# Kernel tuning notes

Measured on AMD Instinct MI355X. Metric: run time of the kernel, lower is better.

## Reference

```python
import jax, jax.numpy as jnp
import numpy as np
import math

FS, N_FFT, NUM_BANDS, NUM_BINS = 16000, 512, 31, 257
H = 96  # dim_hidden

def band_partition():
    f_min, f_max = FS / N_FFT, FS / 2.0
    z_min = 69.0 + 12.0 * math.log2(f_min / 440.0)
    z_max = 69.0 + 12.0 * math.log2(f_max / 440.0)
    z = np.linspace(z_min, z_max, NUM_BANDS + 2)
    f_points = 440.0 * 2.0 ** ((z - 69.0) / 12.0)
    bins = np.round(f_points * N_FFT / FS).astype(np.int64)
    bins[0] = 0
    bands = []
    for i in range(NUM_BANDS):
        s = max(0, int(bins[i]))
        e = min(NUM_BINS, int(bins[i + 2]) + 1)
        if e <= s:
            e = s + 1
        bands.append((s, e))
    return bands

BANDS = band_partition()

def hann(L):
    # torch.hann_window default (periodic=True)
    return 0.5 - 0.5 * jnp.cos(2.0 * jnp.pi * jnp.arange(L, dtype=jnp.float32) / L)

def chan_ln(x, eps=1e-5):
    # AdaNorm2d assumed = LayerNorm over channel dim, no affine
    m = jnp.mean(x, axis=1, keepdims=True)
    v = jnp.var(x, axis=1, keepdims=True)
    return (x - m) * jax.lax.rsqrt(v + eps)

def prelu(x, a):
    return jnp.where(x >= 0, x, a * x)

def setup_inputs() -> dict:
    key = jax.random.key(0)
    ks = jax.random.split(key, 20)
    B, T = 4, 1000
    return {
        'mix_repr': jax.random.normal(ks[0], (B, H, NUM_BINS, T), jnp.float32),
        'spin': jax.random.normal(ks[1], (B, 64, NUM_BINS, T), jnp.float32),
        'doa': jax.random.normal(ks[2], (B, 36), jnp.float32),
        'enc_w': jax.random.normal(ks[3], (NUM_BANDS, H, 64), jnp.float32) * 0.05,
        'enc_b': jax.random.normal(ks[4], (NUM_BANDS, H), jnp.float32) * 0.05,
        'enc_a': 0.25 * jnp.ones((NUM_BANDS,), jnp.float32),
        'dqg_w': jax.random.normal(ks[5], (NUM_BANDS, 2 * H, 36), jnp.float32) * 0.05,
        'dqg_b': jax.random.normal(ks[6], (NUM_BANDS, 2 * H), jnp.float32) * 0.05,
        'dec_w': jax.random.normal(ks[7], (NUM_BANDS, H, H), jnp.float32) * 0.05,
        'dec_b': jax.random.normal(ks[8], (NUM_BANDS, H), jnp.float32) * 0.05,
        'dec_a': 0.25 * jnp.ones((NUM_BANDS,), jnp.float32),
        'qw': jax.random.normal(ks[9], (H, H), jnp.float32) * 0.05,
        'qb': jax.random.normal(ks[10], (H,), jnp.float32) * 0.05,
        'kw': jax.random.normal(ks[11], (H, H), jnp.float32) * 0.05,
        'kb': jax.random.normal(ks[12], (H,), jnp.float32) * 0.05,
        'vw': jax.random.normal(ks[13], (H, H), jnp.float32) * 0.05,
        'vb': jax.random.normal(ks[14], (H,), jnp.float32) * 0.05,
        'ow': jax.random.normal(ks[15], (H, H), jnp.float32) * 0.05,
        'ob': jax.random.normal(ks[16], (H,), jnp.float32) * 0.05,
    }

def reference(mix_repr, spin, doa, enc_w, enc_b, enc_a, dqg_w, dqg_b,
              dec_w, dec_b, dec_a, qw, qb, kw, kb, vw, vb, ow, ob):
    B, D, F, T = mix_repr.shape
    merged = jnp.zeros((B, H, F, T), mix_repr.dtype)
    wsum = jnp.zeros((F,), mix_repr.dtype)
    for k, (s, e) in enumerate(BANDS):  # fixed set of 31 static ragged bands
        L = e - s
        win = hann(L)
        sub = spin[:, :, s:e, :]                                   # [B,64,L,T]
        feat = jnp.einsum('oc,bcft->boft', enc_w[k], sub) + enc_b[k][None, :, None, None]
        feat = prelu(chan_ln(feat), enc_a[k])
        qp = doa @ dqg_w[k].T + dqg_b[k]                           # [B,2H]
        gamma, beta = qp[:, :H], qp[:, H:]
        tgt = (1.0 + gamma)[:, :, None, None] * feat + beta[:, :, None, None]
        dec = jnp.einsum('oc,bcft->boft', dec_w[k], tgt) + dec_b[k][None, :, None, None]
        dec = prelu(chan_ln(dec), dec_a[k])
        merged = merged.at[:, :, s:e, :].add(dec * win[None, None, :, None])
        wsum = wsum.at[s:e].add(win)
    merged = merged / jnp.clip(wsum, 1e-8)[None, None, :, None]
    # MixtureQueryFusion: 1x1 conv cross-attention gate
    Q = jnp.einsum('oc,bcft->boft', qw, mix_repr) + qb[None, :, None, None]
    K = jnp.einsum('oc,bcft->boft', kw, merged) + kb[None, :, None, None]
    V = jnp.einsum('oc,bcft->boft', vw, merged) + vb[None, :, None, None]
    attn = jax.nn.sigmoid(jnp.sum(Q * K, axis=1, keepdims=True) / jnp.sqrt(jnp.float32(H)))
    attended = V * attn
    out = mix_repr + jnp.einsum('oc,bcft->boft', ow, attended) + ob[None, :, None, None]
    return out
```

## Files before the change

### kernel.cpp

```cpp
#include <hip/hip_runtime.h>
#include <math.h>

#define NBANDS 31
#define FT 257000

typedef __attribute__((ext_vector_type(8))) short bh8;
typedef __attribute__((ext_vector_type(4))) float f4;

__constant__ int d_bs[NBANDS] = {0,1,1,2,2,2,3,3,4,5,6,7,8,10,11,13,16,19,23,27,32,38,45,54,64,76,91,108,128,152,181};
__constant__ int d_be[NBANDS] = {2,3,3,3,4,4,5,6,7,8,9,11,12,14,17,20,24,28,33,39,46,55,65,77,92,109,129,153,182,216,257};

__device__ __forceinline__ unsigned short b16u(float v) {
  __bf16 h = (__bf16)v;
  return __builtin_bit_cast(unsigned short, h);
}
__device__ __forceinline__ unsigned pk2(float a, float b) {
  return (unsigned)b16u(a) | ((unsigned)b16u(b) << 16);
}
__device__ __forceinline__ float hann1(int i, int L) {
  return 0.5f - 0.5f * cosf(6.283185307179586f * (float)i / (float)L);
}

__global__ __launch_bounds__(256) void prep_w(
    const float* __restrict__ enc_w, const float* __restrict__ dec_w,
    const float* __restrict__ qw, const float* __restrict__ kw,
    const float* __restrict__ vw, const float* __restrict__ ow,
    unsigned short* __restrict__ w16) {
  const int stride = gridDim.x * blockDim.x;
  for (int i = blockIdx.x * blockDim.x + threadIdx.x; i < 513024; i += stride) {
    float v;
    if (i < 190464) {
      const int k = i / 6144, r = i - k * 6144;
      const int tile = r >> 9, li = r & 511;
      const int lane = li >> 3, j = li & 7;
      const int g = lane >> 4, n = lane & 15;
      const int mt = tile >> 1, kt = tile & 1;
      v = enc_w[k * 6144 + (mt * 16 + n) * 64 + kt * 32 + g * 8 + j];
    } else if (i < 476160) {
      const int i2 = i - 190464;
      const int k = i2 / 9216, r = i2 - k * 9216;
      const int tile = r >> 9, li = r & 511;
      const int lane = li >> 3, j = li & 7;
      const int g = lane >> 4, n = lane & 15;
      const int mt = tile / 3, kt = tile - mt * 3;
      v = dec_w[k * 9216 + (mt * 16 + n) * 96 + kt * 32 + g * 8 + j];
    } else {
      const int i2 = i - 476160;
      const int a = i2 / 9216, r = i2 - a * 9216;
      const int tile = r >> 9, li = r & 511;
      const int lane = li >> 3, j = li & 7;
      const int g = lane >> 4, n = lane & 15;
      const int mt = tile / 3, kt = tile - mt * 3;
      const float* src = (a == 0) ? qw : (a == 1) ? kw : (a == 2) ? vw : ow;
      v = src[(mt * 16 + n) * 96 + kt * 32 + g * 8 + j];
    }
    w16[i] = b16u(v);
  }
}

__global__ __launch_bounds__(192) void qp_kernel(const float* __restrict__ doa,
                                                 const float* __restrict__ dqg_w,
                                                 const float* __restrict__ dqg_b,
                                                 float* __restrict__ gbuf) {
  const int k = blockIdx.x, b = blockIdx.y;
  const int tid = threadIdx.x;
  __shared__ float sdoa[36];
  if (tid < 36) sdoa[tid] = doa[b * 36 + tid];
  __syncthreads();
  const float* wr = dqg_w + (k * 192 + tid) * 36;
  float acc = dqg_b[k * 192 + tid];
  #pragma unroll
  for (int i = 0; i < 36; ++i) acc = fmaf(wr[i], sdoa[i], acc);
  if (tid < 96) acc += 1.0f;
  gbuf[(k * 4 + b) * 192 + tid] = acc;
}

__global__ __launch_bounds__(320) void tab_kernel(float* __restrict__ ftab) {
  const int f = blockIdx.x * blockDim.x + threadIdx.x;
  if (f >= 257) return;
  int k0 = 0; while (d_be[k0] <= f) ++k0;
  int k1 = k0; while (k1 < NBANDS && d_bs[k1] <= f) ++k1;
  float wsum = 0.f, wn[5];
  for (int k = k0; k < k1; ++k) {
    const float wv = hann1(f - d_bs[k], d_be[k] - d_bs[k]);
    wn[k - k0] = wv; wsum += wv;
  }
  float* o = ftab + f * 8;
  o[0] = (float)k0; o[1] = (float)(k1 - k0); o[2] = 1.0f / fmaxf(wsum, 1e-8f);
  #pragma unroll
  for (int j = 0; j < 5; ++j) o[3 + j] = (j < k1 - k0) ? wn[j] : 0.f;
}

#define LDSWAIT asm volatile("s_waitcnt lgkmcnt(0)" ::: "memory")

__device__ __forceinline__ void init6(f4* acc, const float* s, int off) {
  #pragma unroll
  for (int mt = 0; mt < 6; ++mt) {
    const float4 bb = *reinterpret_cast<const float4*>(s + mt * 16 + off);
    acc[mt] = (f4){bb.x, bb.y, bb.z, bb.w};
  }
}
__device__ __forceinline__ void ln96(const f4* acc, float& mean, float& rs) {
  float s0 = 0.f, s1 = 0.f, s2 = 0.f, s3 = 0.f;
  float q0 = 0.f, q1 = 0.f, q2 = 0.f, q3 = 0.f;
  #pragma unroll
  for (int mt = 0; mt < 6; ++mt) {
    const float a0 = acc[mt][0], a1 = acc[mt][1], a2 = acc[mt][2], a3 = acc[mt][3];
    s0 += a0; s1 += a1; s2 += a2; s3 += a3;
    q0 = fmaf(a0, a0, q0); q1 = fmaf(a1, a1, q1);
    q2 = fmaf(a2, a2, q2); q3 = fmaf(a3, a3, q3);
  }
  float sm = (s0 + s1) + (s2 + s3);
  float sq = (q0 + q1) + (q2 + q3);
  sm += __shfl_xor(sm, 16); sm += __shfl_xor(sm, 32);
  sq += __shfl_xor(sq, 16); sq += __shfl_xor(sq, 32);
  mean = sm * (1.f / 96.f);
  rs = rsqrtf(sq * (1.f / 96.f) - mean * mean + 1e-5f);
}
__device__ __forceinline__ void load6s(bh8* dst, const unsigned short* p, int step9) {
  #pragma unroll
  for (int mt = 0; mt < 6; ++mt)
    dst[mt] = *reinterpret_cast<const bh8*>(p + ((mt * step9) << 9));
}

__global__ __launch_bounds__(256, 3) void fused_mfma(
    const float* __restrict__ mix, const float* __restrict__ spin,
    const unsigned short* __restrict__ enc16, const float* __restrict__ enc_b, const float* __restrict__ enc_a,
    const unsigned short* __restrict__ dec16, const float* __restrict__ dec_b, const float* __restrict__ dec_a,
    const float* __restrict__ gb, const float* __restrict__ ftab,
    const unsigned short* __restrict__ q16, const float* __restrict__ qb,
    const unsigned short* __restrict__ k16, const float* __restrict__ kb,
    const unsigned short* __restrict__ v16, const float* __restrict__ vb,
    const unsigned short* __restrict__ o16, const float* __restrict__ ob,
    float* __restrict__ out) {
  const int id0 = (int)blockIdx.x;
  const int id  = (id0 & 7) * 2056 + (id0 >> 3);
  const int tt  = id & 15;
  const int fb  = id >> 4;
  const int f   = fb % 257;
  const int b   = fb / 257;
  const int t0  = tt << 6;

  const int tid  = threadIdx.x;
  const int lane = tid & 63;
  const int w    = tid >> 6;
  const int g    = lane >> 4;
  const int n    = lane & 15;
  const int col  = (w << 4) + n;
  const int t    = t0 + col;
  const int tcl  = (t < 1000) ? t : 999;
  const int sw   = (n & 7) << 3;
  const int lb   = lane << 3;

  __shared__ __align__(16) char smem[28160];
  unsigned short* XT = (unsigned short*)smem;
  float* stage = (float*)(smem + 16384);
  float* OS = (float*)smem;
  unsigned short* xw = XT + col * 128;

  const float* ft = ftab + f * 8;
  const int k0 = (int)ft[0];
  const int nb = (int)ft[1];
  const float winv = ft[2];

  {
    const int tot = (nb << 9) + 384;
    for (int i = tid; i < tot; i += 256) {
      const int kk = i >> 9, r = i & 511;
      float v = 0.f;
      if (kk < nb) {
        const int k = k0 + kk;
        if      (r < 96)  v = enc_b[k * 96 + r];
        else if (r < 192) v = dec_b[k * 96 + (r - 96)];
        else if (r < 384) v = gb[(k * 4 + b) * 192 + (r - 192)];
        else if (r == 384) v = enc_a[k];
        else if (r == 385) v = dec_a[k];
        else if (r == 386) v = ft[3 + kk];
      } else {
        const int r2 = i - (nb << 9);
        v = (r2 < 96) ? qb[r2] : (r2 < 192) ? kb[r2 - 96] : (r2 < 288) ? vb[r2 - 192] : ob[r2 - 288];
      }
      stage[i] = v;
    }
  }

  const float* spL = spin + b * 64 * FT + f * 1000 + tcl;
  const float* mxL = mix  + b * 96 * FT + f * 1000 + tcl;

  bh8 spb[2];
  {
    float spf[16];
    #pragma unroll
    for (int j = 0; j < 8; ++j) spf[j]     = __builtin_nontemporal_load(spL + (g * 8 + j) * FT);
    #pragma unroll
    for (int j = 0; j < 8; ++j) spf[8 + j] = __builtin_nontemporal_load(spL + (32 + g * 8 + j) * FT);
    #pragma unroll
    for (int kt = 0; kt < 2; ++kt)
      #pragma unroll
      for (int j = 0; j < 8; ++j) spb[kt][j] = (short)b16u(spf[kt * 8 + j]);
  }

  bh8 pre[6];
  load6s(pre, enc16 + k0 * 6144 + lb, 2);

  __syncthreads();

  f4 macc[6];
  #pragma unroll
  for (int mt = 0; mt < 6; ++mt) macc[mt] = (f4){0.f, 0.f, 0.f, 0.f};

  const int oo = g * 4;

  for (int kk = 0; kk < nb; ++kk) {
    const int k = k0 + kk;
    const unsigned short* ew  = enc16 + k * 6144 + lb;
    const unsigned short* dwp = dec16 + k * 9216 + lb;
    const float* stg = stage + (kk << 9);

    f4 acc[6];
    init6(acc, stg, oo);
    #pragma unroll
    for (int mt = 0; mt < 6; ++mt)
      acc[mt] = __builtin_amdgcn_mfma_f32_16x16x32_bf16(pre[mt], spb[0], acc[mt], 0, 0, 0);
    #pragma unroll
    for (int mt = 0; mt < 6; ++mt) {
      const bh8 af = *reinterpret_cast<const bh8*>(ew + ((mt * 2 + 1) << 9));
      acc[mt] = __builtin_amdgcn_mfma_f32_16x16x32_bf16(af, spb[1], acc[mt], 0, 0, 0);
    }

    load6s(pre, dwp, 3);

    float mean, rs;
    ln96(acc, mean, rs);
    const float ea = stg[384];
    #pragma unroll
    for (int mt = 0; mt < 6; ++mt) {
      const float4 ga = *reinterpret_cast<const float4*>(stg + 192 + mt * 16 + oo);
      const float4 be = *reinterpret_cast<const float4*>(stg + 288 + mt * 16 + oo);
      float x0 = (acc[mt][0] - mean) * rs; x0 = (x0 >= 0.f) ? x0 : ea * x0;
      float x1 = (acc[mt][1] - mean) * rs; x1 = (x1 >= 0.f) ? x1 : ea * x1;
      float x2 = (acc[mt][2] - mean) * rs; x2 = (x2 >= 0.f) ? x2 : ea * x2;
      float x3 = (acc[mt][3] - mean) * rs; x3 = (x3 >= 0.f) ? x3 : ea * x3;
      uint2 u;
      u.x = pk2(fmaf(ga.x, x0, be.x), fmaf(ga.y, x1, be.y));
      u.y = pk2(fmaf(ga.z, x2, be.z), fmaf(ga.w, x3, be.w));
      *reinterpret_cast<uint2*>(xw + ((mt * 16 + g * 4) ^ sw)) = u;
    }
    LDSWAIT;

    f4 dacc[6];
    init6(dacc, stg + 96, oo);
    {
      const bh8 bf0 = *reinterpret_cast<const bh8*>(xw + ((0 * 32 + g * 8) ^ sw));
      #pragma unroll
      for (int mt = 0; mt < 6; ++mt)
        dacc[mt] = __builtin_amdgcn_mfma_f32_16x16x32_bf16(pre[mt], bf0, dacc[mt], 0, 0, 0);
    }

    {
      const bool more = (kk + 1 < nb);
      load6s(pre, more ? (enc16 + (k + 1) * 6144 + lb) : (q16 + lb), more ? 2 : 3);
    }

    #pragma unroll
    for (int kt = 1; kt < 3; ++kt) {
      const bh8 bf = *reinterpret_cast<const bh8*>(xw + ((kt * 32 + g * 8) ^ sw));
      #pragma unroll
      for (int mt = 0; mt < 6; ++mt) {
        const bh8 af = *reinterpret_cast<const bh8*>(dwp + ((mt * 3 + kt) << 9));
        dacc[mt] = __builtin_amdgcn_mfma_f32_16x16x32_bf16(af, bf, dacc[mt], 0, 0, 0);
      }
    }
    float mean2, rs2;
    ln96(dacc, mean2, rs2);
    const float da = stg[385];
    const float win = stg[386];
    #pragma unroll
    for (int mt = 0; mt < 6; ++mt)
      #pragma unroll
      for (int r = 0; r < 4; ++r) {
        float x = (dacc[mt][r] - mean2) * rs2;
        x = (x >= 0.f) ? x : da * x;
        macc[mt][r] = fmaf(win, x, macc[mt][r]);
      }
  }

  float mxf[24];
  #pragma unroll
  for (int kt = 0; kt < 3; ++kt)
    #pragma unroll
    for (int j = 0; j < 8; ++j) mxf[kt * 8 + j] = mxL[(kt * 32 + g * 8 + j) * FT];

  #pragma unroll
  for (int mt = 0; mt < 6; ++mt) {
    uint2 u;
    u.x = pk2(macc[mt][0] * winv, macc[mt][1] * winv);
    u.y = pk2(macc[mt][2] * winv, macc[mt][3] * winv);
    *reinterpret_cast<uint2*>(xw + ((mt * 16 + g * 4) ^ sw)) = u;
  }
  LDSWAIT;
  bh8 gfr[3];
  #pragma unroll
  for (int kt = 0; kt < 3; ++kt) gfr[kt] = *reinterpret_cast<const bh8*>(xw + ((kt * 32 + g * 8) ^ sw));

  bh8 mxb[3];
  #pragma unroll
  for (int kt = 0; kt < 3; ++kt)
    #pragma unroll
    for (int j = 0; j < 8; ++j) mxb[kt][j] = (short)b16u(mxf[kt * 8 + j]);

  const float* stQ = stage + (nb << 9);

  f4 qacc[6];
  init6(qacc, stQ, oo);
  const unsigned short* qp16 = q16 + lb;
  #pragma unroll
  for (int mt = 0; mt < 6; ++mt)
    qacc[mt] = __builtin_amdgcn_mfma_f32_16x16x32_bf16(pre[mt], mxb[0], qacc[mt], 0, 0, 0);
  load6s(pre, k16 + lb, 3);
  #pragma unroll
  for (int kt = 1; kt < 3; ++kt)
    #pragma unroll
    for (int mt = 0; mt < 6; ++mt) {
      const bh8 af = *reinterpret_cast<const bh8*>(qp16 + ((mt * 3 + kt) << 9));
      qacc[mt] = __builtin_amdgcn_mfma_f32_16x16x32_bf16(af, mxb[kt], qacc[mt], 0, 0, 0);
    }
  f4 kacc[6];
  init6(kacc, stQ + 96, oo);
  const unsigned short* kp16 = k16 + lb;
  #pragma unroll
  for (int mt = 0; mt < 6; ++mt)
    kacc[mt] = __builtin_amdgcn_mfma_f32_16x16x32_bf16(pre[mt], gfr[0], kacc[mt], 0, 0, 0);
  load6s(pre, v16 + lb, 3);
  #pragma unroll
  for (int kt = 1; kt < 3; ++kt)
    #pragma unroll
    for (int mt = 0; mt < 6; ++mt) {
      const bh8 af = *reinterpret_cast<const bh8*>(kp16 + ((mt * 3 + kt) << 9));
      kacc[mt] = __builtin_amdgcn_mfma_f32_16x16x32_bf16(af, gfr[kt], kacc[mt], 0, 0, 0);
    }
  float p0 = 0.f, p1 = 0.f;
  #pragma unroll
  for (int mt = 0; mt < 6; ++mt) {
    p0 = fmaf(qacc[mt][0], kacc[mt][0], p0);
    p1 = fmaf(qacc[mt][1], kacc[mt][1], p1);
    p0 = fmaf(qacc[mt][2], kacc[mt][2], p0);
    p1 = fmaf(qacc[mt][3], kacc[mt][3], p1);
  }
  float p = p0 + p1;
  p += __shfl_xor(p, 16); p += __shfl_xor(p, 32);
  const float sig = 1.f / (1.f + __expf(-p * 0.10206207261596575f));

  f4 vacc[6];
  init6(vacc, stQ + 192, oo);
  const unsigned short* vp16 = v16 + lb;
  #pragma unroll
  for (int mt = 0; mt < 6; ++mt)
    vacc[mt] = __builtin_amdgcn_mfma_f32_16x16x32_bf16(pre[mt], gfr[0], vacc[mt], 0, 0, 0);
  load6s(pre, o16 + lb, 3);
  #pragma unroll
  for (int kt = 1; kt < 3; ++kt)
    #pragma unroll
    for (int mt = 0; mt < 6; ++mt) {
      const bh8 af = *reinterpret_cast<const bh8*>(vp16 + ((mt * 3 + kt) << 9));
      vacc[mt] = __builtin_amdgcn_mfma_f32_16x16x32_bf16(af, gfr[kt], vacc[mt], 0, 0, 0);
    }
  #pragma unroll
  for (int mt = 0; mt < 6; ++mt) {
    uint2 u;
    u.x = pk2(vacc[mt][0] * sig, vacc[mt][1] * sig);
    u.y = pk2(vacc[mt][2] * sig, vacc[mt][3] * sig);
    *reinterpret_cast<uint2*>(xw + ((mt * 16 + g * 4) ^ sw)) = u;
  }
  LDSWAIT;
  bh8 afr[3];
  #pragma unroll
  for (int kt = 0; kt < 3; ++kt) afr[kt] = *reinterpret_cast<const bh8*>(xw + ((kt * 32 + g * 8) ^ sw));

  f4 oacc[6];
  init6(oacc, stQ + 288, oo);
  const unsigned short* op16 = o16 + lb;
  #pragma unroll
  for (int mt = 0; mt < 6; ++mt)
    oacc[mt] = __builtin_amdgcn_mfma_f32_16x16x32_bf16(pre[mt], afr[0], oacc[mt], 0, 0, 0);
  #pragma unroll
  for (int kt = 1; kt < 3; ++kt)
    #pragma unroll
    for (int mt = 0; mt < 6; ++mt) {
      const bh8 af = *reinterpret_cast<const bh8*>(op16 + ((mt * 3 + kt) << 9));
      oacc[mt] = __builtin_amdgcn_mfma_f32_16x16x32_bf16(af, afr[kt], oacc[mt], 0, 0, 0);
    }

  __syncthreads();

  #pragma unroll
  for (int mt = 0; mt < 6; ++mt)
    #pragma unroll
    for (int r = 0; r < 4; ++r)
      OS[(mt * 16 + g * 4 + r) * 65 + col] = oacc[mt][r];

  __syncthreads();

  const int cvalid = 1000 - t0;
  #pragma unroll
  for (int it = 0; it < 24; ++it) {
    const int i   = it * 256 + tid;
    const int row = i >> 6;
    const int c   = i & 63;
    if (c < cvalid) {
      const long gi = (long)(b * 96 + row) * FT + f * 1000 + t0 + c;
      const float val = OS[row * 65 + c] + mix[gi];
      __builtin_nontemporal_store(val, out + gi);
    }
  }
}

extern "C" void kernel_launch(void* const* d_in, const int* in_sizes, int n_in,
                              void* d_out, int out_size, void* d_ws, size_t ws_size,
                              hipStream_t stream) {
  (void)in_sizes; (void)n_in; (void)out_size; (void)ws_size;
  const float* mix   = (const float*)d_in[0];
  const float* spin  = (const float*)d_in[1];
  const float* doa   = (const float*)d_in[2];
  const float* enc_w = (const float*)d_in[3];
  const float* enc_b = (const float*)d_in[4];
  const float* enc_a = (const float*)d_in[5];
  const float* dqg_w = (const float*)d_in[6];
  const float* dqg_b = (const float*)d_in[7];
  const float* dec_w = (const float*)d_in[8];
  const float* dec_b = (const float*)d_in[9];
  const float* dec_a = (const float*)d_in[10];
  const float* qw    = (const float*)d_in[11];
  const float* qb    = (const float*)d_in[12];
  const float* kw    = (const float*)d_in[13];
  const float* kb    = (const float*)d_in[14];
  const float* vw    = (const float*)d_in[15];
  const float* vb    = (const float*)d_in[16];
  const float* oww   = (const float*)d_in[17];
  const float* obb   = (const float*)d_in[18];
  float* outp = (float*)d_out;

  unsigned short* w16 = (unsigned short*)d_ws;
  unsigned short* enc16 = w16;
  unsigned short* dec16 = w16 + 190464;
  unsigned short* q16   = w16 + 476160;
  unsigned short* k16   = q16 + 9216;
  unsigned short* v16   = k16 + 9216;
  unsigned short* o16   = v16 + 9216;
  float* gbws = (float*)((char*)d_ws + 1026048);
  float* ftab = (float*)((char*)d_ws + 1121280);

  hipLaunchKernelGGL(prep_w, dim3(512), dim3(256), 0, stream,
                     enc_w, dec_w, qw, kw, vw, oww, w16);
  hipLaunchKernelGGL(qp_kernel, dim3(NBANDS, 4), dim3(192), 0, stream,
                     doa, dqg_w, dqg_b, gbws);
  hipLaunchKernelGGL(tab_kernel, dim3(1), dim3(320), 0, stream, ftab);
  hipLaunchKernelGGL(fused_mfma, dim3(16448), dim3(256), 0, stream,
                     mix, spin, enc16, enc_b, enc_a, dec16, dec_b, dec_a, gbws, ftab,
                     q16, qb, k16, kb, v16, vb, o16, obb, outp);
}
```

Baseline: 544.3 us.

## Fold FiLM gamma/beta into per-batch decoder weights and vectorize output epilogue

Adds a prep kernel that multiplies the decoder weights by gamma and folds beta into the decoder bias for each (band, batch), so the fused kernel no longer applies the FiLM modulation per element. This shrinks the per-band staging area in LDS and removes the gamma/beta loads and FMAs from the inner loop. The cost is four times as many decoder weight copies in workspace, which means less cache reuse of weights. The output epilogue also switches to float4 loads and stores with a padded LDS stride for full tiles, cutting the number of memory instructions.

```diff
diff --git a/kernel.cpp b/kernel.cpp
--- a/kernel.cpp
+++ b/kernel.cpp
@@ -6,6 +6,7 @@
 
 typedef __attribute__((ext_vector_type(8))) short bh8;
 typedef __attribute__((ext_vector_type(4))) float f4;
+typedef __attribute__((ext_vector_type(4))) float f4v;
 
 __constant__ int d_bs[NBANDS] = {0,1,1,2,2,2,3,3,4,5,6,7,8,10,11,13,16,19,23,27,32,38,45,54,64,76,91,108,128,152,181};
 __constant__ int d_be[NBANDS] = {2,3,3,3,4,4,5,6,7,8,9,11,12,14,17,20,24,28,33,39,46,55,65,77,92,109,129,153,182,216,257};
@@ -75,6 +76,29 @@
   gbuf[(k * 4 + b) * 192 + tid] = acc;
 }
 
+__global__ __launch_bounds__(96) void prep_dec(
+    const float* __restrict__ dec_w, const float* __restrict__ dec_b,
+    const float* __restrict__ gbuf,
+    unsigned short* __restrict__ dec16b, float* __restrict__ decBb) {
+  const int k = blockIdx.x, b = blockIdx.y;
+  const int o = threadIdx.x;
+  __shared__ float gm[96], bt[96];
+  gm[o] = gbuf[(k * 4 + b) * 192 + o];
+  bt[o] = gbuf[(k * 4 + b) * 192 + 96 + o];
+  __syncthreads();
+  const float* wr = dec_w + k * 9216 + o * 96;
+  float bias = dec_b[k * 96 + o];
+  unsigned short* dst = dec16b + (b * 31 + k) * 9216;
+  const int mt = o >> 4, n = o & 15;
+  for (int c = 0; c < 96; ++c) {
+    const float wv = wr[c];
+    bias = fmaf(wv, bt[c], bias);
+    const int kt = c >> 5, g = (c & 31) >> 3, j = c & 7;
+    dst[((mt * 3 + kt) << 9) + (((g << 4) + n) << 3) + j] = b16u(wv * gm[c]);
+  }
+  decBb[(b * 31 + k) * 96 + o] = bias;
+}
+
 __global__ __launch_bounds__(320) void tab_kernel(float* __restrict__ ftab) {
   const int f = blockIdx.x * blockDim.x + threadIdx.x;
   if (f >= 257) return;
@@ -126,8 +150,8 @@
 __global__ __launch_bounds__(256, 3) void fused_mfma(
     const float* __restrict__ mix, const float* __restrict__ spin,
     const unsigned short* __restrict__ enc16, const float* __restrict__ enc_b, const float* __restrict__ enc_a,
-    const unsigned short* __restrict__ dec16, const float* __restrict__ dec_b, const float* __restrict__ dec_a,
-    const float* __restrict__ gb, const float* __restrict__ ftab,
+    const unsigned short* __restrict__ dec16b, const float* __restrict__ decBb, const float* __restrict__ dec_a,
+    const float* __restrict__ ftab,
     const unsigned short* __restrict__ q16, const float* __restrict__ qb,
     const unsigned short* __restrict__ k16, const float* __restrict__ kb,
     const unsigned short* __restrict__ v16, const float* __restrict__ vb,
@@ -151,8 +175,9 @@
   const int tcl  = (t < 1000) ? t : 999;
   const int sw   = (n & 7) << 3;
   const int lb   = lane << 3;
-
-  __shared__ __align__(16) char smem[28160];
+  const int bk   = b * 31;
+
+  __shared__ __align__(16) char smem[26112];
   unsigned short* XT = (unsigned short*)smem;
   float* stage = (float*)(smem + 16384);
   float* OS = (float*)smem;
@@ -164,20 +189,19 @@
   const float winv = ft[2];
 
   {
-    const int tot = (nb << 9) + 384;
+    const int tot = (nb << 8) + 384;
     for (int i = tid; i < tot; i += 256) {
-      const int kk = i >> 9, r = i & 511;
+      const int kk = i >> 8, r = i & 255;
       float v = 0.f;
       if (kk < nb) {
         const int k = k0 + kk;
         if      (r < 96)  v = enc_b[k * 96 + r];
-        else if (r < 192) v = dec_b[k * 96 + (r - 96)];
-        else if (r < 384) v = gb[(k * 4 + b) * 192 + (r - 192)];
-        else if (r == 384) v = enc_a[k];
-        else if (r == 385) v = dec_a[k];
-        else if (r == 386) v = ft[3 + kk];
+        else if (r < 192) v = decBb[(bk + k) * 96 + (r - 96)];
+        else if (r == 192) v = enc_a[k];
+        else if (r == 193) v = dec_a[k];
+        else if (r == 194) v = ft[3 + kk];
       } else {
-        const int r2 = i - (nb << 9);
+        const int r2 = i - (nb << 8);
         v = (r2 < 96) ? qb[r2] : (r2 < 192) ? kb[r2 - 96] : (r2 < 288) ? vb[r2 - 192] : ob[r2 - 288];
       }
       stage[i] = v;
@@ -214,8 +238,8 @@
   for (int kk = 0; kk < nb; ++kk) {
     const int k = k0 + kk;
     const unsigned short* ew  = enc16 + k * 6144 + lb;
-    const unsigned short* dwp = dec16 + k * 9216 + lb;
-    const float* stg = stage + (kk << 9);
+    const unsigned short* dwp = dec16b + (bk + k) * 9216 + lb;
+    const float* stg = stage + (kk << 8);
 
     f4 acc[6];
     init6(acc, stg, oo);
@@ -232,19 +256,17 @@
 
     float mean, rs;
     ln96(acc, mean, rs);
-    const float ea = stg[384];
-    #pragma unroll
-    for (int mt = 0; mt < 6; ++mt) {
-      const float4 ga = *reinterpret_cast<const float4*>(stg + 192 + mt * 16 + oo);
-      const float4 be = *reinterpret_cast<const float4*>(stg + 288 + mt * 16 + oo);
+    const float ea = stg[192];
+    #pragma unroll
+    for (int mt = 0; mt < 6; ++mt) {
       float x0 = (acc[mt][0] - mean) * rs; x0 = (x0 >= 0.f) ? x0 : ea * x0;
       float x1 = (acc[mt][1] - mean) * rs; x1 = (x1 >= 0.f) ? x1 : ea * x1;
       float x2 = (acc[mt][2] - mean) * rs; x2 = (x2 >= 0.f) ? x2 : ea * x2;
       float x3 = (acc[mt][3] - mean) * rs; x3 = (x3 >= 0.f) ? x3 : ea * x3;
       uint2 u;
-      u.x = pk2(fmaf(ga.x, x0, be.x), fmaf(ga.y, x1, be.y));
-      u.y = pk2(fmaf(ga.z, x2, be.z), fmaf(ga.w, x3, be.w));
-      *reinterpret_cast<uint2*>(xw + ((mt * 16 + g * 4) ^ sw)) = u;
+      u.x = pk2(x0, x1);
+      u.y = pk2(x2, x3);
+      *reinterpret_cast<uint2*>(xw + ((mt * 16 + oo) ^ sw)) = u;
     }
     LDSWAIT;
 
@@ -273,8 +295,8 @@
     }
     float mean2, rs2;
     ln96(dacc, mean2, rs2);
-    const float da = stg[385];
-    const float win = stg[386];
+    const float da = stg[193];
+    const float win = stg[194];
     #pragma unroll
     for (int mt = 0; mt < 6; ++mt)
       #pragma unroll
@@ -296,7 +318,7 @@
     uint2 u;
     u.x = pk2(macc[mt][0] * winv, macc[mt][1] * winv);
     u.y = pk2(macc[mt][2] * winv, macc[mt][3] * winv);
-    *reinterpret_cast<uint2*>(xw + ((mt * 16 + g * 4) ^ sw)) = u;
+    *reinterpret_cast<uint2*>(xw + ((mt * 16 + oo) ^ sw)) = u;
   }
   LDSWAIT;
   bh8 gfr[3];
@@ -309,7 +331,7 @@
     #pragma unroll
     for (int j = 0; j < 8; ++j) mxb[kt][j] = (short)b16u(mxf[kt * 8 + j]);
 
-  const float* stQ = stage + (nb << 9);
+  const float* stQ = stage + (nb << 8);
 
   f4 qacc[6];
   init6(qacc, stQ, oo);
@@ -370,7 +392,7 @@
     uint2 u;
     u.x = pk2(vacc[mt][0] * sig, vacc[mt][1] * sig);
     u.y = pk2(vacc[mt][2] * sig, vacc[mt][3] * sig);
-    *reinterpret_cast<uint2*>(xw + ((mt * 16 + g * 4) ^ sw)) = u;
+    *reinterpret_cast<uint2*>(xw + ((mt * 16 + oo) ^ sw)) = u;
   }
   LDSWAIT;
   bh8 afr[3];
@@ -397,20 +419,33 @@
   for (int mt = 0; mt < 6; ++mt)
     #pragma unroll
     for (int r = 0; r < 4; ++r)
-      OS[(mt * 16 + g * 4 + r) * 65 + col] = oacc[mt][r];
+      OS[(mt * 16 + oo + r) * 68 + col] = oacc[mt][r];
 
   __syncthreads();
 
   const int cvalid = 1000 - t0;
-  #pragma unroll
-  for (int it = 0; it < 24; ++it) {
-    const int i   = it * 256 + tid;
-    const int row = i >> 6;
-    const int c   = i & 63;
-    if (c < cvalid) {
-      const long gi = (long)(b * 96 + row) * FT + f * 1000 + t0 + c;
-      const float val = OS[row * 65 + c] + mix[gi];
-      __builtin_nontemporal_store(val, out + gi);
+  if (cvalid >= 64) {
+    #pragma unroll
+    for (int it = 0; it < 6; ++it) {
+      const int i   = it * 256 + tid;
+      const int row = i >> 4;
+      const int c4  = (i & 15) << 2;
+      f4v v = *reinterpret_cast<const f4v*>(&OS[row * 68 + c4]);
+      const long gi = (long)(b * 96 + row) * FT + f * 1000 + t0 + c4;
+      const f4v m = *reinterpret_cast<const f4v*>(mix + gi);
+      v = v + m;
+      __builtin_nontemporal_store(v, reinterpret_cast<f4v*>(out + gi));
+    }
+  } else {
+    #pragma unroll
+    for (int it = 0; it < 24; ++it) {
+      const int i   = it * 256 + tid;
+      const int row = i >> 6;
+      const int c   = i & 63;
+      if (c < cvalid) {
+        const long gi = (long)(b * 96 + row) * FT + f * 1000 + t0 + c;
+        __builtin_nontemporal_store(OS[row * 68 + c] + mix[gi], out + gi);
+      }
     }
   }
 }
@@ -442,20 +477,23 @@
 
   unsigned short* w16 = (unsigned short*)d_ws;
   unsigned short* enc16 = w16;
-  unsigned short* dec16 = w16 + 190464;
   unsigned short* q16   = w16 + 476160;
   unsigned short* k16   = q16 + 9216;
   unsigned short* v16   = k16 + 9216;
   unsigned short* o16   = v16 + 9216;
   float* gbws = (float*)((char*)d_ws + 1026048);
   float* ftab = (float*)((char*)d_ws + 1121280);
+  unsigned short* dec16b = (unsigned short*)((char*)d_ws + 1129504);
+  float* decBb = (float*)((char*)d_ws + 3415072);
 
   hipLaunchKernelGGL(prep_w, dim3(512), dim3(256), 0, stream,
                      enc_w, dec_w, qw, kw, vw, oww, w16);
   hipLaunchKernelGGL(qp_kernel, dim3(NBANDS, 4), dim3(192), 0, stream,
                      doa, dqg_w, dqg_b, gbws);
+  hipLaunchKernelGGL(prep_dec, dim3(NBANDS, 4), dim3(96), 0, stream,
+                     dec_w, dec_b, gbws, dec16b, decBb);
   hipLaunchKernelGGL(tab_kernel, dim3(1), dim3(320), 0, stream, ftab);
   hipLaunchKernelGGL(fused_mfma, dim3(16448), dim3(256), 0, stream,
-                     mix, spin, enc16, enc_b, enc_a, dec16, dec_b, dec_a, gbws, ftab,
+                     mix, spin, enc16, enc_b, enc_a, dec16b, decBb, dec_a, ftab,
                      q16, qb, k16, kb, v16, vb, o16, obb, outp);
 }
```

After: 545.3 us. No clear change (+0.2%).
